# Kernel optimization log

Measured on AMD Instinct MI355X. Metric: run time of the kernel, lower is better.

The kernel has to match this reference:

```python
import jax, jax.numpy as jnp
import numpy as np

VOCAB = 32000
HIDDEN = 512


def setup_inputs() -> dict:
    key = jax.random.key(0)
    k1, k2, k3, k4 = jax.random.split(key, 4)
    B, L = 64, 2048  # batch of trees, leaves per (complete binary) tree
    leaf_ids = jax.random.randint(k1, (B, L), 0, VOCAB)
    emb = jax.random.normal(k2, (VOCAB, HIDDEN), dtype=jnp.float32)
    # nn.Linear(2H, H): weight [H, 2H], bias [H]
    lim = 1.0 / np.sqrt(2 * HIDDEN)
    W = jax.random.uniform(k3, (HIDDEN, 2 * HIDDEN), minval=-lim, maxval=lim, dtype=jnp.float32)
    b = jax.random.uniform(k4, (HIDDEN,), minval=-lim, maxval=lim, dtype=jnp.float32)
    return {"leaf_ids": leaf_ids, "emb": emb, "W": W, "b": b}


def reference(leaf_ids, emb, W, b):
    # Preterminal nodes: embed leaf token then activation (matches original order).
    h = jnp.tanh(emb[leaf_ids])  # [B, L, H]
    B, L, H = h.shape
    n_levels = int(np.log2(L))
    # Bottom-up: each internal node concatenates its two children -> linear -> tanh.
    # All same-depth nodes processed as one batched GEMM.
    for _ in range(n_levels):
        n = h.shape[1]
        pairs = h.reshape(B, n // 2, 2 * H)          # concat(left, right) along feature dim
        h = jnp.tanh(jnp.einsum('bnf,hf->bnh', pairs, W) + b)
    return h  # [B, 1, H] root hidden state per tree
```

## Files before the change

### kernel.cpp

```cpp
#include <hip/hip_runtime.h>
#include <stdint.h>

typedef __attribute__((ext_vector_type(8))) short short8;
typedef __attribute__((ext_vector_type(4))) float floatx4;

__device__ __forceinline__ unsigned short f2bf(float x) {
    unsigned int u = __builtin_bit_cast(unsigned int, x);
    unsigned int r = (u + 0x7FFFu + ((u >> 16) & 1u)) >> 16;
    return (unsigned short)r;
}

__device__ __forceinline__ float fast_tanh(float x) {
    float xc = fminf(fmaxf(x, -10.0f), 10.0f);
    float e  = __expf(2.0f * xc);
    float d  = e + 1.0f;
    float r  = __builtin_amdgcn_rcpf(d);
    r = r * (2.0f - d * r);
    return (e - 1.0f) * r;
}

__global__ void wconv(const float4* __restrict__ W4, ushort4* __restrict__ Wb4) {
    int i = blockIdx.x * 256 + threadIdx.x;
    float4 v = W4[i];
    ushort4 o;
    o.x = f2bf(v.x); o.y = f2bf(v.y); o.z = f2bf(v.z); o.w = f2bf(v.w);
    Wb4[i] = o;
}

__global__ void tconv(const float4* __restrict__ emb4, ushort4* __restrict__ embT4) {
    int i = blockIdx.x * 256 + threadIdx.x;
    float4 v = emb4[i];
    ushort4 o;
    o.x = f2bf(fast_tanh(v.x)); o.y = f2bf(fast_tanh(v.y));
    o.z = f2bf(fast_tanh(v.z)); o.w = f2bf(fast_tanh(v.w));
    embT4[i] = o;
}

#define STAGE_(sA, sB, Ap, Bp, buf, k0)                                         \
    do {                                                                        \
        __builtin_amdgcn_global_load_lds(                                       \
            (const __attribute__((address_space(1))) void*)((Ap) + (k0)),       \
            (__attribute__((address_space(3))) void*)&sA[buf][tid * 8], 16, 0, 0); \
        __builtin_amdgcn_global_load_lds(                                       \
            (const __attribute__((address_space(1))) void*)((Ap) + 64 * 1024 + (k0)), \
            (__attribute__((address_space(3))) void*)&sA[buf][2048 + tid * 8], 16, 0, 0); \
        __builtin_amdgcn_global_load_lds(                                       \
            (const __attribute__((address_space(1))) void*)((Bp) + (k0)),       \
            (__attribute__((address_space(3))) void*)&sB[buf][tid * 8], 16, 0, 0); \
        __builtin_amdgcn_global_load_lds(                                       \
            (const __attribute__((address_space(1))) void*)((Bp) + 64 * 1024 + (k0)), \
            (__attribute__((address_space(3))) void*)&sB[buf][2048 + tid * 8], 16, 0, 0); \
    } while (0)

#define STAGE_E(sA, sB, buf, k0)                                                \
    do {                                                                        \
        const ushort* sLo_ = ((k0) < 512) ? (a0lo + (k0)) : (a1lo + ((k0) - 512)); \
        const ushort* sHi_ = ((k0) < 512) ? (a0hi + (k0)) : (a1hi + ((k0) - 512)); \
        __builtin_amdgcn_global_load_lds(                                       \
            (const __attribute__((address_space(1))) void*)sLo_,                \
            (__attribute__((address_space(3))) void*)&sA[buf][tid * 8], 16, 0, 0); \
        __builtin_amdgcn_global_load_lds(                                       \
            (const __attribute__((address_space(1))) void*)sHi_,                \
            (__attribute__((address_space(3))) void*)&sA[buf][2048 + tid * 8], 16, 0, 0); \
        __builtin_amdgcn_global_load_lds(                                       \
            (const __attribute__((address_space(1))) void*)(Bp + (k0)),         \
            (__attribute__((address_space(3))) void*)&sB[buf][tid * 8], 16, 0, 0); \
        __builtin_amdgcn_global_load_lds(                                       \
            (const __attribute__((address_space(1))) void*)(Bp + 64 * 1024 + (k0)), \
            (__attribute__((address_space(3))) void*)&sB[buf][2048 + tid * 8], 16, 0, 0); \
    } while (0)

#define COMPUTE_(sA, sB, cur)                                                   \
    do {                                                                        \
        short8 a_[4], b_[4];                                                    \
        _Pragma("unroll")                                                       \
        for (int mi = 0; mi < 4; ++mi)                                          \
            a_[mi] = *reinterpret_cast<const short8*>(&sA[cur][(rA + mi * 16) * 32 + kksw]); \
        _Pragma("unroll")                                                       \
        for (int ni = 0; ni < 4; ++ni)                                          \
            b_[ni] = *reinterpret_cast<const short8*>(&sB[cur][(rB + ni * 16) * 32 + kksw]); \
        __builtin_amdgcn_s_setprio(1);                                          \
        _Pragma("unroll")                                                       \
        for (int mi = 0; mi < 4; ++mi)                                          \
            _Pragma("unroll")                                                   \
            for (int ni = 0; ni < 4; ++ni)                                      \
                acc[mi][ni] = __builtin_amdgcn_mfma_f32_16x16x32_bf16(          \
                    a_[mi], b_[ni], acc[mi][ni], 0, 0, 0);                      \
        __builtin_amdgcn_s_setprio(0);                                          \
    } while (0)

#define KLOOPX_(STG, sA, sB)                                                    \
    do {                                                                        \
        STG(0, 0);                                                              \
        STG(1, 32);                                                             \
        for (int t = 0; t < 30; t += 3) {                                       \
            asm volatile("s_barrier" ::: "memory");                             \
            STG(2, (t + 2) * 32);                                               \
            asm volatile("s_waitcnt vmcnt(4)" ::: "memory");                    \
            COMPUTE_(sA, sB, 0);                                                \
            asm volatile("s_barrier" ::: "memory");                             \
            STG(0, (t + 3) * 32);                                               \
            asm volatile("s_waitcnt vmcnt(4)" ::: "memory");                    \
            COMPUTE_(sA, sB, 1);                                                \
            asm volatile("s_barrier" ::: "memory");                             \
            STG(1, (t + 4) * 32);                                               \
            asm volatile("s_waitcnt vmcnt(4)" ::: "memory");                    \
            COMPUTE_(sA, sB, 2);                                                \
        }                                                                       \
        asm volatile("s_barrier" ::: "memory");                                 \
        asm volatile("s_waitcnt vmcnt(0)" ::: "memory");                        \
        COMPUTE_(sA, sB, 0);                                                    \
        asm volatile("s_barrier" ::: "memory");                                 \
        asm volatile("s_waitcnt vmcnt(0)" ::: "memory");                        \
        COMPUTE_(sA, sB, 1);                                                    \
    } while (0)

#define EPILOGUE_B()                                                            \
    do {                                                                        \
        const int mrow = (lane >> 4) * 4;                                       \
        const int ncol = lane & 15;                                             \
        _Pragma("unroll")                                                       \
        for (int mi = 0; mi < 4; ++mi) {                                        \
            _Pragma("unroll")                                                   \
            for (int ni = 0; ni < 4; ++ni) {                                    \
                const int n = n0 + wc * 64 + ni * 16 + ncol;                    \
                const float bb = bias[n];                                       \
                _Pragma("unroll")                                               \
                for (int j = 0; j < 4; ++j) {                                   \
                    const int m = m0 + wr * 64 + mi * 16 + mrow + j;            \
                    float v = fast_tanh(acc[mi][ni][j] + bb);                   \
                    outb[(size_t)m * 512 + n] = f2bf(v);                        \
                }                                                               \
            }                                                                   \
        }                                                                       \
    } while (0)

__global__ __launch_bounds__(256)
void level1_gemm(const int* __restrict__ ids, const ushort* __restrict__ embT,
                 const ushort* __restrict__ Bt, const float* __restrict__ bias,
                 ushort* __restrict__ outb)
{
    const int nb  = gridDim.x;
    int bid = blockIdx.x;
    const int per = nb >> 3;
    const int lin = (bid & 7) * per + (bid >> 3);
    const int mt = lin >> 2, nt = lin & 3;
    const int m0 = mt * 128, n0 = nt * 128;

    __shared__ alignas(16) ushort sA[3][4096];
    __shared__ alignas(16) ushort sB[3][4096];

    const int tid  = threadIdx.x;
    const int lane = tid & 63;
    const int w    = tid >> 6;
    const int wr   = w >> 1, wc = w & 1;

    const int sr    = tid >> 2;
    const int swcol = (((tid & 3) ^ ((tid >> 3) & 3)) << 3);
    const int mlo = m0 + sr, mhi = m0 + sr + 64;
    const ushort* a0lo = embT + (size_t)ids[2 * mlo]     * 512 + swcol;
    const ushort* a1lo = embT + (size_t)ids[2 * mlo + 1] * 512 + swcol;
    const ushort* a0hi = embT + (size_t)ids[2 * mhi]     * 512 + swcol;
    const ushort* a1hi = embT + (size_t)ids[2 * mhi + 1] * 512 + swcol;
    const ushort* Bp   = Bt + (size_t)(n0 + sr) * 1024 + swcol;

    const int rA   = wr * 64 + (lane & 15);
    const int rB   = wc * 64 + (lane & 15);
    const int kksw = (((lane >> 4) ^ ((lane >> 1) & 3)) << 3);

    floatx4 acc[4][4] = {};
#define STG1(buf, k0) STAGE_E(sA, sB, buf, k0)
    KLOOPX_(STG1, sA, sB);
#undef STG1
    EPILOGUE_B();
}

__global__ __launch_bounds__(256)
void level_gemm(const ushort* __restrict__ A, const ushort* __restrict__ Bt,
                const float* __restrict__ bias,
                ushort* __restrict__ outb, int M)
{
    const int nb  = gridDim.x;
    int bid = blockIdx.x;
    const int per = nb >> 3;
    const int lin = (bid & 7) * per + (bid >> 3);
    const int mt = lin >> 2, nt = lin & 3;
    const int m0 = mt * 128, n0 = nt * 128;

    __shared__ alignas(16) ushort sA[3][4096];
    __shared__ alignas(16) ushort sB[3][4096];

    const int tid  = threadIdx.x;
    const int lane = tid & 63;
    const int w    = tid >> 6;
    const int wr   = w >> 1, wc = w & 1;

    const int sr    = tid >> 2;
    const int swcol = (((tid & 3) ^ ((tid >> 3) & 3)) << 3);
    const ushort* Ap = A  + (size_t)(m0 + sr) * 1024 + swcol;
    const ushort* Bp = Bt + (size_t)(n0 + sr) * 1024 + swcol;

    const int rA   = wr * 64 + (lane & 15);
    const int rB   = wc * 64 + (lane & 15);
    const int kksw = (((lane >> 4) ^ ((lane >> 1) & 3)) << 3);

    floatx4 acc[4][4] = {};
#define STG0(buf, k0) STAGE_(sA, sB, Ap, Bp, buf, k0)
    KLOOPX_(STG0, sA, sB);
#undef STG0
    EPILOGUE_B();
}

__global__ __launch_bounds__(256)
void small_gemm(const ushort* __restrict__ A, const ushort* __restrict__ Bt,
                const float* __restrict__ bias,
                ushort* __restrict__ outb, float* __restrict__ outf, int last)
{
    __shared__ alignas(16) ushort sA[3][4096];
    __shared__ alignas(16) ushort sB[3][4096];

    const int tid  = threadIdx.x;
    const int lane = tid & 63;
    const int w    = tid >> 6;
    const int l15  = lane & 15;
    const int lh   = lane >> 4;
    const int mt   = blockIdx.x >> 3, nt = blockIdx.x & 7;
    const int m0   = mt * 64, n0 = nt * 64;

    const int r0 = tid >> 3;
    const int s0 = tid & 7;
    const int swz = ((s0 ^ (r0 & 7)) << 3);
    const ushort* Ap = A  + (size_t)(m0 + r0) * 1024 + swz;
    const ushort* Bp = Bt + (size_t)(n0 + r0) * 1024 + swz;

#define STG6(buf, k0)                                                           \
    do {                                                                        \
        __builtin_amdgcn_global_load_lds(                                       \
            (const __attribute__((address_space(1))) void*)(Ap + (k0)),         \
            (__attribute__((address_space(3))) void*)&sA[buf][tid * 8], 16, 0, 0); \
        __builtin_amdgcn_global_load_lds(                                       \
            (const __attribute__((address_space(1))) void*)(Ap + 32 * 1024 + (k0)), \
            (__attribute__((address_space(3))) void*)&sA[buf][2048 + tid * 8], 16, 0, 0); \
        __builtin_amdgcn_global_load_lds(                                       \
            (const __attribute__((address_space(1))) void*)(Bp + (k0)),         \
            (__attribute__((address_space(3))) void*)&sB[buf][tid * 8], 16, 0, 0); \
        __builtin_amdgcn_global_load_lds(                                       \
            (const __attribute__((address_space(1))) void*)(Bp + 32 * 1024 + (k0)), \
            (__attribute__((address_space(3))) void*)&sB[buf][2048 + tid * 8], 16, 0, 0); \
    } while (0)

    const int rb = w * 16 + l15;
    floatx4 acc[4] = {};

#define CMP6(buf)                                                               \
    do {                                                                        \
        _Pragma("unroll")                                                       \
        for (int ks = 0; ks < 2; ++ks) {                                        \
            const int kq = ks * 4 + lh;                                         \
            const short8 b_ = *reinterpret_cast<const short8*>(                 \
                &sB[buf][rb * 64 + ((kq ^ (rb & 7)) << 3)]);                    \
            __builtin_amdgcn_s_setprio(1);                                      \
            _Pragma("unroll")                                                   \
            for (int mi = 0; mi < 4; ++mi) {                                    \
                const int ra = mi * 16 + l15;                                   \
                const short8 a_ = *reinterpret_cast<const short8*>(             \
                    &sA[buf][ra * 64 + ((kq ^ (l15 & 7)) << 3)]);               \
                acc[mi] = __builtin_amdgcn_mfma_f32_16x16x32_bf16(              \
                    a_, b_, acc[mi], 0, 0, 0);                                  \
            }                                                                   \
            __builtin_amdgcn_s_setprio(0);                                      \
        }                                                                       \
    } while (0)

    STG6(0, 0);
    STG6(1, 64);
    for (int t3 = 0; t3 < 12; t3 += 3) {
        asm volatile("s_barrier" ::: "memory");
        STG6(2, (t3 + 2) * 64);
        asm volatile("s_waitcnt vmcnt(4)" ::: "memory");
        CMP6(0);
        asm volatile("s_barrier" ::: "memory");
        STG6(0, (t3 + 3) * 64);
        asm volatile("s_waitcnt vmcnt(4)" ::: "memory");
        CMP6(1);
        asm volatile("s_barrier" ::: "memory");
        STG6(1, (t3 + 4) * 64);
        asm volatile("s_waitcnt vmcnt(4)" ::: "memory");
        CMP6(2);
    }
    asm volatile("s_barrier" ::: "memory");
    STG6(2, 14 * 64);
    asm volatile("s_waitcnt vmcnt(8)" ::: "memory");
    CMP6(0);
    asm volatile("s_barrier" ::: "memory");
    STG6(0, 15 * 64);
    asm volatile("s_waitcnt vmcnt(8)" ::: "memory");
    CMP6(1);
    asm volatile("s_barrier" ::: "memory");
    asm volatile("s_waitcnt vmcnt(4)" ::: "memory");
    CMP6(2);
    asm volatile("s_barrier" ::: "memory");
    asm volatile("s_waitcnt vmcnt(0)" ::: "memory");
    CMP6(0);
#undef CMP6
#undef STG6

    const int n  = n0 + w * 16 + l15;
    const float bb = bias[n];
    #pragma unroll
    for (int mi = 0; mi < 4; ++mi) {
        #pragma unroll
        for (int j = 0; j < 4; ++j) {
            const int m = m0 + mi * 16 + lh * 4 + j;
            float v = fast_tanh(acc[mi][j] + bb);
            if (last) outf[(size_t)m * 512 + n] = v;
            else      outb[(size_t)m * 512 + n] = f2bf(v);
        }
    }
}

extern "C" void kernel_launch(void* const* d_in, const int* in_sizes, int n_in,
                              void* d_out, int out_size, void* d_ws, size_t ws_size,
                              hipStream_t stream) {
    const int*   ids  = (const int*)d_in[0];
    const float* emb  = (const float*)d_in[1];
    const float* W    = (const float*)d_in[2];
    const float* bias = (const float*)d_in[3];
    float* out = (float*)d_out;

    unsigned short* Wb   = (unsigned short*)d_ws;
    unsigned short* embT = Wb + 524288;
    unsigned short* hB   = embT + 16384000;
    unsigned short* hA   = hB + 33554432;

    wconv<<<512, 256, 0, stream>>>((const float4*)W, (ushort4*)Wb);
    tconv<<<16000, 256, 0, stream>>>((const float4*)emb, (ushort4*)embT);

    level1_gemm<<<2048, 256, 0, stream>>>(ids, embT, Wb, bias, hB);

    int M = 32768;
    for (int l = 2; l <= 4; ++l) {
        const unsigned short* in = (l & 1) ? hA : hB;
        unsigned short*       ob = (l & 1) ? hB : hA;
        level_gemm<<<(M / 128) * 4, 256, 0, stream>>>(in, Wb, bias, ob, M);
        M >>= 1;
    }
    for (int l = 5; l <= 11; ++l) {
        const unsigned short* in = (l & 1) ? hA : hB;
        unsigned short*       ob = (l & 1) ? hB : hA;
        small_gemm<<<(M / 64) * 8, 256, 0, stream>>>(in, Wb, bias, ob, out,
                                                     l == 11 ? 1 : 0);
        M >>= 1;
    }
}
```

Measured before the change: 292.0 us.

## Precompute per-vocab left/right projections for level one, then gather-add

Level one is now computed by projecting the whole embedding table through the left and right halves of W once (two 32000x512 tables, 16 K-steps each). A separate elementwise kernel then gathers the rows for each leaf pair, adds them with the bias and applies tanh. This replaces the gathered 32768-row, K=1024 GEMM with a 32000-row, K=512 GEMM per half plus a cheap gather pass. In exchange it writes and re-reads about 65 MB of intermediate bf16 projections, and adds a bf16 rounding step on the partial sums before they are added.

```diff
diff --git a/kernel.cpp b/kernel.cpp
--- a/kernel.cpp
+++ b/kernel.cpp
@@ -8,6 +8,10 @@
     unsigned int u = __builtin_bit_cast(unsigned int, x);
     unsigned int r = (u + 0x7FFFu + ((u >> 16) & 1u)) >> 16;
     return (unsigned short)r;
+}
+__device__ __forceinline__ float bf2f(unsigned short x) {
+    unsigned int u = ((unsigned int)x) << 16;
+    return __builtin_bit_cast(float, u);
 }
 
 __device__ __forceinline__ float fast_tanh(float x) {
@@ -52,21 +56,19 @@
             (__attribute__((address_space(3))) void*)&sB[buf][2048 + tid * 8], 16, 0, 0); \
     } while (0)
 
-#define STAGE_E(sA, sB, buf, k0)                                                \
-    do {                                                                        \
-        const ushort* sLo_ = ((k0) < 512) ? (a0lo + (k0)) : (a1lo + ((k0) - 512)); \
-        const ushort* sHi_ = ((k0) < 512) ? (a0hi + (k0)) : (a1hi + ((k0) - 512)); \
-        __builtin_amdgcn_global_load_lds(                                       \
-            (const __attribute__((address_space(1))) void*)sLo_,                \
+#define STAGE_PQ(sA, sB, Ap, Bp, buf, k0)                                       \
+    do {                                                                        \
+        __builtin_amdgcn_global_load_lds(                                       \
+            (const __attribute__((address_space(1))) void*)((Ap) + (k0)),       \
             (__attribute__((address_space(3))) void*)&sA[buf][tid * 8], 16, 0, 0); \
         __builtin_amdgcn_global_load_lds(                                       \
-            (const __attribute__((address_space(1))) void*)sHi_,                \
+            (const __attribute__((address_space(1))) void*)((Ap) + 64 * 512 + (k0)), \
             (__attribute__((address_space(3))) void*)&sA[buf][2048 + tid * 8], 16, 0, 0); \
         __builtin_amdgcn_global_load_lds(                                       \
-            (const __attribute__((address_space(1))) void*)(Bp + (k0)),         \
+            (const __attribute__((address_space(1))) void*)((Bp) + (k0)),       \
             (__attribute__((address_space(3))) void*)&sB[buf][tid * 8], 16, 0, 0); \
         __builtin_amdgcn_global_load_lds(                                       \
-            (const __attribute__((address_space(1))) void*)(Bp + 64 * 1024 + (k0)), \
+            (const __attribute__((address_space(1))) void*)((Bp) + 64 * 1024 + (k0)), \
             (__attribute__((address_space(3))) void*)&sB[buf][2048 + tid * 8], 16, 0, 0); \
     } while (0)
 
@@ -89,62 +91,32 @@
         __builtin_amdgcn_s_setprio(0);                                          \
     } while (0)
 
-#define KLOOPX_(STG, sA, sB)                                                    \
-    do {                                                                        \
-        STG(0, 0);                                                              \
-        STG(1, 32);                                                             \
-        for (int t = 0; t < 30; t += 3) {                                       \
-            asm volatile("s_barrier" ::: "memory");                             \
-            STG(2, (t + 2) * 32);                                               \
-            asm volatile("s_waitcnt vmcnt(4)" ::: "memory");                    \
-            COMPUTE_(sA, sB, 0);                                                \
-            asm volatile("s_barrier" ::: "memory");                             \
-            STG(0, (t + 3) * 32);                                               \
-            asm volatile("s_waitcnt vmcnt(4)" ::: "memory");                    \
-            COMPUTE_(sA, sB, 1);                                                \
-            asm volatile("s_barrier" ::: "memory");                             \
-            STG(1, (t + 4) * 32);                                               \
-            asm volatile("s_waitcnt vmcnt(4)" ::: "memory");                    \
-            COMPUTE_(sA, sB, 2);                                                \
-        }                                                                       \
+#define ITER_S_(STG, sA, sB, cur, stg, tile)                                    \
+    do {                                                                        \
+        asm volatile("s_barrier" ::: "memory");                                 \
+        STG(sA, sB, Ap, Bp, stg, (tile) * 32);                                  \
+        asm volatile("s_waitcnt vmcnt(4)" ::: "memory");                        \
+        COMPUTE_(sA, sB, cur);                                                  \
+    } while (0)
+
+#define ITER_D_(sA, sB, cur)                                                    \
+    do {                                                                        \
         asm volatile("s_barrier" ::: "memory");                                 \
         asm volatile("s_waitcnt vmcnt(0)" ::: "memory");                        \
-        COMPUTE_(sA, sB, 0);                                                    \
-        asm volatile("s_barrier" ::: "memory");                                 \
-        asm volatile("s_waitcnt vmcnt(0)" ::: "memory");                        \
-        COMPUTE_(sA, sB, 1);                                                    \
-    } while (0)
-
-#define EPILOGUE_B()                                                            \
-    do {                                                                        \
-        const int mrow = (lane >> 4) * 4;                                       \
-        const int ncol = lane & 15;                                             \
-        _Pragma("unroll")                                                       \
-        for (int mi = 0; mi < 4; ++mi) {                                        \
-            _Pragma("unroll")                                                   \
-            for (int ni = 0; ni < 4; ++ni) {                                    \
-                const int n = n0 + wc * 64 + ni * 16 + ncol;                    \
-                const float bb = bias[n];                                       \
-                _Pragma("unroll")                                               \
-                for (int j = 0; j < 4; ++j) {                                   \
-                    const int m = m0 + wr * 64 + mi * 16 + mrow + j;            \
-                    float v = fast_tanh(acc[mi][ni][j] + bb);                   \
-                    outb[(size_t)m * 512 + n] = f2bf(v);                        \
-                }                                                               \
-            }                                                                   \
-        }                                                                       \
+        COMPUTE_(sA, sB, cur);                                                  \
     } while (0)
 
 __global__ __launch_bounds__(256)
-void level1_gemm(const int* __restrict__ ids, const ushort* __restrict__ embT,
-                 const ushort* __restrict__ Bt, const float* __restrict__ bias,
-                 ushort* __restrict__ outb)
+void pq_gemm(const ushort* __restrict__ embT, const ushort* __restrict__ Bt,
+             ushort* __restrict__ PQ)
 {
     const int nb  = gridDim.x;
     int bid = blockIdx.x;
     const int per = nb >> 3;
     const int lin = (bid & 7) * per + (bid >> 3);
-    const int mt = lin >> 2, nt = lin & 3;
+    const int table = lin / 1000;
+    const int rem   = lin - table * 1000;
+    const int mt = rem >> 2, nt = rem & 3;
     const int m0 = mt * 128, n0 = nt * 128;
 
     __shared__ alignas(16) ushort sA[3][4096];
@@ -157,22 +129,64 @@
 
     const int sr    = tid >> 2;
     const int swcol = (((tid & 3) ^ ((tid >> 3) & 3)) << 3);
-    const int mlo = m0 + sr, mhi = m0 + sr + 64;
-    const ushort* a0lo = embT + (size_t)ids[2 * mlo]     * 512 + swcol;
-    const ushort* a1lo = embT + (size_t)ids[2 * mlo + 1] * 512 + swcol;
-    const ushort* a0hi = embT + (size_t)ids[2 * mhi]     * 512 + swcol;
-    const ushort* a1hi = embT + (size_t)ids[2 * mhi + 1] * 512 + swcol;
-    const ushort* Bp   = Bt + (size_t)(n0 + sr) * 1024 + swcol;
+    const ushort* Ap = embT + (size_t)(m0 + sr) * 512 + swcol;
+    const ushort* Bp = Bt + (size_t)(n0 + sr) * 1024 + (table << 9) + swcol;
 
     const int rA   = wr * 64 + (lane & 15);
     const int rB   = wc * 64 + (lane & 15);
     const int kksw = (((lane >> 4) ^ ((lane >> 1) & 3)) << 3);
 
     floatx4 acc[4][4] = {};
-#define STG1(buf, k0) STAGE_E(sA, sB, buf, k0)
-    KLOOPX_(STG1, sA, sB);
-#undef STG1
-    EPILOGUE_B();
+
+    STAGE_PQ(sA, sB, Ap, Bp, 0, 0);
+    STAGE_PQ(sA, sB, Ap, Bp, 1, 32);
+    for (int t = 0; t < 12; t += 3) {
+        ITER_S_(STAGE_PQ, sA, sB, 0, 2, t + 2);
+        ITER_S_(STAGE_PQ, sA, sB, 1, 0, t + 3);
+        ITER_S_(STAGE_PQ, sA, sB, 2, 1, t + 4);
+    }
+    ITER_S_(STAGE_PQ, sA, sB, 0, 2, 14);
+    ITER_S_(STAGE_PQ, sA, sB, 1, 0, 15);
+    ITER_D_(sA, sB, 2);
+    ITER_D_(sA, sB, 0);
+
+    ushort* outp = PQ + (size_t)table * 16384000;
+    const int mrow = (lane >> 4) * 4;
+    const int ncol = lane & 15;
+    #pragma unroll
+    for (int mi = 0; mi < 4; ++mi)
+        #pragma unroll
+        for (int ni = 0; ni < 4; ++ni) {
+            const int n = n0 + wc * 64 + ni * 16 + ncol;
+            #pragma unroll
+            for (int j = 0; j < 4; ++j) {
+                const int m = m0 + wr * 64 + mi * 16 + mrow + j;
+                outp[(size_t)m * 512 + n] = f2bf(acc[mi][ni][j]);
+            }
+        }
+}
+
+__global__ void lvl1_add(const int* __restrict__ ids, const ushort* __restrict__ PQ,
+                         const float* __restrict__ bias, ushort* __restrict__ h1)
+{
+    int idx = blockIdx.x * 256 + threadIdx.x;
+    int m = idx >> 6;
+    int c = (idx & 63) << 3;
+    const int il = ids[2 * m], ir = ids[2 * m + 1];
+    const short8 p = *reinterpret_cast<const short8*>(PQ + (size_t)il * 512 + c);
+    const short8 q = *reinterpret_cast<const short8*>(PQ + 16384000 + (size_t)ir * 512 + c);
+    const float4 b0 = *reinterpret_cast<const float4*>(bias + c);
+    const float4 b1 = *reinterpret_cast<const float4*>(bias + c + 4);
+    short8 o;
+    o[0] = (short)f2bf(fast_tanh(bf2f((unsigned short)p[0]) + bf2f((unsigned short)q[0]) + b0.x));
+    o[1] = (short)f2bf(fast_tanh(bf2f((unsigned short)p[1]) + bf2f((unsigned short)q[1]) + b0.y));
+    o[2] = (short)f2bf(fast_tanh(bf2f((unsigned short)p[2]) + bf2f((unsigned short)q[2]) + b0.z));
+    o[3] = (short)f2bf(fast_tanh(bf2f((unsigned short)p[3]) + bf2f((unsigned short)q[3]) + b0.w));
+    o[4] = (short)f2bf(fast_tanh(bf2f((unsigned short)p[4]) + bf2f((unsigned short)q[4]) + b1.x));
+    o[5] = (short)f2bf(fast_tanh(bf2f((unsigned short)p[5]) + bf2f((unsigned short)q[5]) + b1.y));
+    o[6] = (short)f2bf(fast_tanh(bf2f((unsigned short)p[6]) + bf2f((unsigned short)q[6]) + b1.z));
+    o[7] = (short)f2bf(fast_tanh(bf2f((unsigned short)p[7]) + bf2f((unsigned short)q[7]) + b1.w));
+    *reinterpret_cast<short8*>(h1 + (size_t)idx * 8) = o;
 }
 
 __global__ __launch_bounds__(256)
@@ -205,10 +219,32 @@
     const int kksw = (((lane >> 4) ^ ((lane >> 1) & 3)) << 3);
 
     floatx4 acc[4][4] = {};
-#define STG0(buf, k0) STAGE_(sA, sB, Ap, Bp, buf, k0)
-    KLOOPX_(STG0, sA, sB);
-#undef STG0
-    EPILOGUE_B();
+
+    STAGE_(sA, sB, Ap, Bp, 0, 0);
+    STAGE_(sA, sB, Ap, Bp, 1, 32);
+    for (int t = 0; t < 30; t += 3) {
+        ITER_S_(STAGE_, sA, sB, 0, 2, t + 2);
+        ITER_S_(STAGE_, sA, sB, 1, 0, t + 3);
+        ITER_S_(STAGE_, sA, sB, 2, 1, t + 4);
+    }
+    ITER_D_(sA, sB, 0);
+    ITER_D_(sA, sB, 1);
+
+    const int mrow = (lane >> 4) * 4;
+    const int ncol = lane & 15;
+    #pragma unroll
+    for (int mi = 0; mi < 4; ++mi)
+        #pragma unroll
+        for (int ni = 0; ni < 4; ++ni) {
+            const int n = n0 + wc * 64 + ni * 16 + ncol;
+            const float bb = bias[n];
+            #pragma unroll
+            for (int j = 0; j < 4; ++j) {
+                const int m = m0 + wr * 64 + mi * 16 + mrow + j;
+                float v = fast_tanh(acc[mi][ni][j] + bb);
+                outb[(size_t)m * 512 + n] = f2bf(v);
+            }
+        }
 }
 
 __global__ __launch_bounds__(256)
@@ -330,13 +366,15 @@
 
     unsigned short* Wb   = (unsigned short*)d_ws;
     unsigned short* embT = Wb + 524288;
-    unsigned short* hB   = embT + 16384000;
+    unsigned short* PQ   = embT + 16384000;
+    unsigned short* hB   = PQ + 32768000;
     unsigned short* hA   = hB + 33554432;
 
     wconv<<<512, 256, 0, stream>>>((const float4*)W, (ushort4*)Wb);
     tconv<<<16000, 256, 0, stream>>>((const float4*)emb, (ushort4*)embT);
 
-    level1_gemm<<<2048, 256, 0, stream>>>(ids, embT, Wb, bias, hB);
+    pq_gemm<<<2000, 256, 0, stream>>>(embT, Wb, PQ);
+    lvl1_add<<<16384, 256, 0, stream>>>(ids, PQ, bias, hB);
 
     int M = 32768;
     for (int l = 2; l <= 4; ++l) {
```

Result: faster. 274.2 us (-6.1%).
